# Kernel tuning notes

Measured on AMD Instinct MI355X. Metric: run time of the kernel, lower is better.

## Reference

```python
import jax, jax.numpy as jnp
import numpy as np

E, N, D = 800000, 50000, 64

def setup_inputs() -> dict:
    key = jax.random.key(0)
    k0, k1, k2, k3 = jax.random.split(key, 4)
    return {
        "edge_attrs": jax.random.normal(k0, (E, D), dtype=jnp.float32),
        "proj_W": jax.random.normal(k1, (D, D), dtype=jnp.float32) / np.float32(np.sqrt(D)),
        "proj_b": jnp.zeros((D,), dtype=jnp.float32),
        "upd_W": jax.random.normal(k2, (D, D), dtype=jnp.float32) / np.float32(np.sqrt(D)),
        "upd_b": jnp.zeros((D,), dtype=jnp.float32),
        "dst": jax.random.randint(k3, (E,), 0, N, dtype=jnp.int32),
        "n_nodes": N,
    }

def reference(edge_attrs, proj_W, proj_b, upd_W, upd_b, dst, n_nodes):
    # Project each edge attribute: node_projectors[e.type](e.data)
    proj = edge_attrs @ proj_W + proj_b                      # [E, D]
    # Mean-aggregate incoming edges per destination node (MeanAggregator)
    summed = jax.ops.segment_sum(proj, dst, num_segments=n_nodes)          # [N, D]
    counts = jax.ops.segment_sum(jnp.ones((dst.shape[0], 1), proj.dtype),
                                 dst, num_segments=n_nodes)                # [N, 1]
    aggregated = summed / jnp.maximum(counts, 1.0)           # nodes w/o edges -> 0
    # Per-node update: updaters(aggregated)
    return aggregated @ upd_W + upd_b                        # [N, D]
```

## Files before the change

kernel.cpp:

```cpp
#include <hip/hip_runtime.h>
#include <hip/hip_bf16.h>

#define D 64

__global__ void zero_kernel(int* __restrict__ p, int n) {
    int i = blockIdx.x * blockDim.x + threadIdx.x;
    if (i < n) p[i] = 0;
}

__global__ void count_kernel(const int* __restrict__ dst, int* __restrict__ counts, int E) {
    int e = blockIdx.x * blockDim.x + threadIdx.x;
    if (e < E) atomicAdd(&counts[dst[e]], 1);
}

__global__ void scan_kernel(const int* __restrict__ counts, int* __restrict__ offsets,
                            int* __restrict__ cursor, int N) {
    __shared__ int wsum[16];
    int t = threadIdx.x;
    int wave = t >> 6, lane = t & 63;
    int carry = 0;
    for (int base = 0; base < N; base += 1024) {
        int i = base + t;
        int v = (i < N) ? counts[i] : 0;
        int s = v;
        #pragma unroll
        for (int off = 1; off < 64; off <<= 1) {
            int x = __shfl_up(s, off);
            if (lane >= off) s += x;
        }
        if (lane == 63) wsum[wave] = s;
        __syncthreads();
        int wbase = 0, total = 0;
        #pragma unroll
        for (int w = 0; w < 16; ++w) {
            int x = wsum[w];
            total += x;
            if (w < wave) wbase += x;
        }
        int incl = s + wbase + carry;
        int excl = incl - v;
        if (i < N) { offsets[i] = excl; cursor[i] = excl; }
        carry += total;
        __syncthreads();
    }
    if (t == 0) offsets[N] = carry;
}

__global__ void fill_kernel(const int* __restrict__ dst, int* __restrict__ cursor,
                            int* __restrict__ csr, int E) {
    int e = blockIdx.x * blockDim.x + threadIdx.x;
    if (e < E) {
        int pos = atomicAdd(&cursor[dst[e]], 1);
        csr[pos] = e;
    }
}

__global__ void combine_kernel(const float* __restrict__ Wp, const float* __restrict__ Wu,
                               const float* __restrict__ bp, float* __restrict__ Wc,
                               float* __restrict__ bc) {
    int idx = blockIdx.x * blockDim.x + threadIdx.x;
    int d = idx >> 6, j = idx & 63;
    float s = 0.f;
    #pragma unroll
    for (int k = 0; k < D; ++k) s = fmaf(Wp[d * D + k], Wu[k * D + j], s);
    Wc[idx] = s;
    if (d == 0) {
        float t = 0.f;
        #pragma unroll
        for (int k = 0; k < D; ++k) t = fmaf(bp[k], Wu[k * D + j], t);
        bc[j] = t;
    }
}

__global__ __launch_bounds__(256) void node_kernel(
        const float* __restrict__ attrs, const int* __restrict__ csr,
        const int* __restrict__ offsets,
        const float* __restrict__ Wc, const float* __restrict__ bc,
        const float* __restrict__ ub, float* __restrict__ out, int N) {
    __shared__ float wlds[D * D];
    __shared__ float blds[D];
    __shared__ float ulds[D];
    int t = threadIdx.x;
    #pragma unroll
    for (int i = t; i < D * D; i += 256) wlds[i] = Wc[i];
    if (t < D) { blds[t] = bc[t]; ulds[t] = ub[t]; }
    __syncthreads();

    int wave = t >> 6, lane = t & 63;
    int n = blockIdx.x * 4 + wave;
    if (n >= N) return;

    int off = offsets[n];
    int cnt = offsets[n + 1] - off;

    float sum = 0.f;
    for (int base = 0; base < cnt; base += 64) {
        int m = cnt - base; if (m > 64) m = 64;
        int idxv = (lane < m) ? csr[off + base + lane] : 0;
        int jj = 0;
        for (; jj + 8 <= m; jj += 8) {
            int e0 = __shfl(idxv, jj + 0);
            int e1 = __shfl(idxv, jj + 1);
            int e2 = __shfl(idxv, jj + 2);
            int e3 = __shfl(idxv, jj + 3);
            int e4 = __shfl(idxv, jj + 4);
            int e5 = __shfl(idxv, jj + 5);
            int e6 = __shfl(idxv, jj + 6);
            int e7 = __shfl(idxv, jj + 7);
            float a0 = attrs[(size_t)e0 * D + lane];
            float a1 = attrs[(size_t)e1 * D + lane];
            float a2 = attrs[(size_t)e2 * D + lane];
            float a3 = attrs[(size_t)e3 * D + lane];
            float a4 = attrs[(size_t)e4 * D + lane];
            float a5 = attrs[(size_t)e5 * D + lane];
            float a6 = attrs[(size_t)e6 * D + lane];
            float a7 = attrs[(size_t)e7 * D + lane];
            sum += ((a0 + a1) + (a2 + a3)) + ((a4 + a5) + (a6 + a7));
        }
        for (; jj < m; ++jj) {
            int e = __shfl(idxv, jj);
            sum += attrs[(size_t)e * D + lane];
        }
    }

    float mean = (cnt > 0) ? sum / (float)cnt : 0.f;
    float acc = ulds[lane] + ((cnt > 0) ? blds[lane] : 0.f);
    #pragma unroll
    for (int d = 0; d < D; ++d) {
        float m = __shfl(mean, d);
        acc = fmaf(m, wlds[d * D + lane], acc);
    }
    out[(size_t)n * D + lane] = acc;
}

extern "C" void kernel_launch(void* const* d_in, const int* in_sizes, int n_in,
                              void* d_out, int out_size, void* d_ws, size_t ws_size,
                              hipStream_t stream) {
    const float* edge_attrs = (const float*)d_in[0];
    const float* proj_W     = (const float*)d_in[1];
    const float* proj_b     = (const float*)d_in[2];
    const float* upd_W      = (const float*)d_in[3];
    const float* upd_b      = (const float*)d_in[4];
    const int*   dst        = (const int*)d_in[5];

    const int E = in_sizes[0] / D;
    const int N = out_size / D;

    int*   counts  = (int*)d_ws;
    int*   offsets = counts + N;
    int*   cursor  = offsets + N + 1;
    int*   csr     = cursor + N;
    float* Wc      = (float*)(csr + E);
    float* bc      = Wc + D * D;

    zero_kernel<<<(N + 255) / 256, 256, 0, stream>>>(counts, N);

    int blocks_e = (E + 255) / 256;
    count_kernel<<<blocks_e, 256, 0, stream>>>(dst, counts, E);
    scan_kernel<<<1, 1024, 0, stream>>>(counts, offsets, cursor, N);
    fill_kernel<<<blocks_e, 256, 0, stream>>>(dst, cursor, csr, E);
    combine_kernel<<<16, 256, 0, stream>>>(proj_W, upd_W, proj_b, Wc, bc);

    int blocks_n = (N + 3) / 4;
    node_kernel<<<blocks_n, 256, 0, stream>>>(edge_attrs, csr, offsets,
                                              Wc, bc, upd_b, (float*)d_out, N);
}
```

Baseline: 211.4 us.

## Parallelize prefix scan across blocks and gather edges with float4 loads

The single-block serial scan over 50k counts becomes a three-kernel scheme: per-block sums, a scan of those block sums, then a per-block scan that adds the block offset. This spreads the scan across the GPU instead of running it as a long serial loop in one workgroup. The node gather now has each quarter-wave read a whole edge row as float4, so four edges are processed per iteration, and partial sums are combined with xor shuffles. The cost is two extra kernel launches and a cross-lane reduction, with no unroll-by-8 left in the gather.

```diff
diff --git a/kernel.cpp b/kernel.cpp
--- a/kernel.cpp
+++ b/kernel.cpp
@@ -13,37 +13,64 @@
     if (e < E) atomicAdd(&counts[dst[e]], 1);
 }
 
-__global__ void scan_kernel(const int* __restrict__ counts, int* __restrict__ offsets,
-                            int* __restrict__ cursor, int N) {
+__global__ void blocksum_kernel(const int* __restrict__ counts, int* __restrict__ bsums, int N) {
+    int t = threadIdx.x;
+    int i = blockIdx.x * 256 + t;
+    int v = (i < N) ? counts[i] : 0;
+    int lane = t & 63, wave = t >> 6;
+    #pragma unroll
+    for (int o = 1; o < 64; o <<= 1) v += __shfl_xor(v, o);
+    __shared__ int ws[4];
+    if (lane == 0) ws[wave] = v;
+    __syncthreads();
+    if (t == 0) bsums[blockIdx.x] = ws[0] + ws[1] + ws[2] + ws[3];
+}
+
+__global__ void blockscan_kernel(const int* __restrict__ bsums, int* __restrict__ boffs,
+                                 int* __restrict__ offsets, int N, int nb) {
     __shared__ int wsum[16];
     int t = threadIdx.x;
     int wave = t >> 6, lane = t & 63;
-    int carry = 0;
-    for (int base = 0; base < N; base += 1024) {
-        int i = base + t;
-        int v = (i < N) ? counts[i] : 0;
-        int s = v;
-        #pragma unroll
-        for (int off = 1; off < 64; off <<= 1) {
-            int x = __shfl_up(s, off);
-            if (lane >= off) s += x;
-        }
-        if (lane == 63) wsum[wave] = s;
-        __syncthreads();
-        int wbase = 0, total = 0;
-        #pragma unroll
-        for (int w = 0; w < 16; ++w) {
-            int x = wsum[w];
-            total += x;
-            if (w < wave) wbase += x;
-        }
-        int incl = s + wbase + carry;
-        int excl = incl - v;
-        if (i < N) { offsets[i] = excl; cursor[i] = excl; }
-        carry += total;
-        __syncthreads();
+    int v = (t < nb) ? bsums[t] : 0;
+    int s = v;
+    #pragma unroll
+    for (int off = 1; off < 64; off <<= 1) {
+        int x = __shfl_up(s, off);
+        if (lane >= off) s += x;
     }
-    if (t == 0) offsets[N] = carry;
+    if (lane == 63) wsum[wave] = s;
+    __syncthreads();
+    int wbase = 0, total = 0;
+    #pragma unroll
+    for (int w = 0; w < 16; ++w) {
+        int x = wsum[w];
+        total += x;
+        if (w < wave) wbase += x;
+    }
+    if (t < nb) boffs[t] = s - v + wbase;
+    if (t == 0) offsets[N] = total;
+}
+
+__global__ void scatter_scan_kernel(const int* __restrict__ counts, const int* __restrict__ boffs,
+                                    int* __restrict__ offsets, int* __restrict__ cursor, int N) {
+    int t = threadIdx.x;
+    int i = blockIdx.x * 256 + t;
+    int v = (i < N) ? counts[i] : 0;
+    int lane = t & 63, wave = t >> 6;
+    int s = v;
+    #pragma unroll
+    for (int off = 1; off < 64; off <<= 1) {
+        int x = __shfl_up(s, off);
+        if (lane >= off) s += x;
+    }
+    __shared__ int ws[4];
+    if (lane == 63) ws[wave] = s;
+    __syncthreads();
+    int wbase = 0;
+    #pragma unroll
+    for (int w = 0; w < 4; ++w) if (w < wave) wbase += ws[w];
+    int excl = s - v + wbase + boffs[blockIdx.x];
+    if (i < N) { offsets[i] = excl; cursor[i] = excl; }
 }
 
 __global__ void fill_kernel(const int* __restrict__ dst, int* __restrict__ cursor,
@@ -73,7 +100,7 @@
 }
 
 __global__ __launch_bounds__(256) void node_kernel(
-        const float* __restrict__ attrs, const int* __restrict__ csr,
+        const float4* __restrict__ attrs4, const int* __restrict__ csr,
         const int* __restrict__ offsets,
         const float* __restrict__ Wc, const float* __restrict__ bc,
         const float* __restrict__ ub, float* __restrict__ out, int N) {
@@ -93,44 +120,37 @@
     int off = offsets[n];
     int cnt = offsets[n + 1] - off;
 
-    float sum = 0.f;
+    int g = lane >> 4;
+    int q = lane & 15;
+
+    float4 acc = make_float4(0.f, 0.f, 0.f, 0.f);
     for (int base = 0; base < cnt; base += 64) {
         int m = cnt - base; if (m > 64) m = 64;
         int idxv = (lane < m) ? csr[off + base + lane] : 0;
-        int jj = 0;
-        for (; jj + 8 <= m; jj += 8) {
-            int e0 = __shfl(idxv, jj + 0);
-            int e1 = __shfl(idxv, jj + 1);
-            int e2 = __shfl(idxv, jj + 2);
-            int e3 = __shfl(idxv, jj + 3);
-            int e4 = __shfl(idxv, jj + 4);
-            int e5 = __shfl(idxv, jj + 5);
-            int e6 = __shfl(idxv, jj + 6);
-            int e7 = __shfl(idxv, jj + 7);
-            float a0 = attrs[(size_t)e0 * D + lane];
-            float a1 = attrs[(size_t)e1 * D + lane];
-            float a2 = attrs[(size_t)e2 * D + lane];
-            float a3 = attrs[(size_t)e3 * D + lane];
-            float a4 = attrs[(size_t)e4 * D + lane];
-            float a5 = attrs[(size_t)e5 * D + lane];
-            float a6 = attrs[(size_t)e6 * D + lane];
-            float a7 = attrs[(size_t)e7 * D + lane];
-            sum += ((a0 + a1) + (a2 + a3)) + ((a4 + a5) + (a6 + a7));
-        }
-        for (; jj < m; ++jj) {
-            int e = __shfl(idxv, jj);
-            sum += attrs[(size_t)e * D + lane];
+        for (int jj = 0; jj < m; jj += 4) {
+            int sel = jj + g;
+            int e = __shfl(idxv, sel);
+            if (sel < m) {
+                float4 a = attrs4[(size_t)e * 16 + q];
+                acc.x += a.x; acc.y += a.y; acc.z += a.z; acc.w += a.w;
+            }
         }
     }
+    acc.x += __shfl_xor(acc.x, 16); acc.y += __shfl_xor(acc.y, 16);
+    acc.z += __shfl_xor(acc.z, 16); acc.w += __shfl_xor(acc.w, 16);
+    acc.x += __shfl_xor(acc.x, 32); acc.y += __shfl_xor(acc.y, 32);
+    acc.z += __shfl_xor(acc.z, 32); acc.w += __shfl_xor(acc.w, 32);
 
-    float mean = (cnt > 0) ? sum / (float)cnt : 0.f;
-    float acc = ulds[lane] + ((cnt > 0) ? blds[lane] : 0.f);
+    float inv = (cnt > 0) ? 1.f / (float)cnt : 0.f;
+    float marr[4] = { acc.x * inv, acc.y * inv, acc.z * inv, acc.w * inv };
+
+    float accO = ulds[lane] + ((cnt > 0) ? blds[lane] : 0.f);
     #pragma unroll
     for (int d = 0; d < D; ++d) {
-        float m = __shfl(mean, d);
-        acc = fmaf(m, wlds[d * D + lane], acc);
+        float mv = __shfl(marr[d & 3], d >> 2);
+        accO = fmaf(mv, wlds[d * D + lane], accO);
     }
-    out[(size_t)n * D + lane] = acc;
+    out[(size_t)n * D + lane] = accO;
 }
 
 extern "C" void kernel_launch(void* const* d_in, const int* in_sizes, int n_in,
@@ -145,11 +165,14 @@
 
     const int E = in_sizes[0] / D;
     const int N = out_size / D;
+    const int nb = (N + 255) / 256;
 
     int*   counts  = (int*)d_ws;
     int*   offsets = counts + N;
     int*   cursor  = offsets + N + 1;
-    int*   csr     = cursor + N;
+    int*   bsums   = cursor + N;
+    int*   boffs   = bsums + nb;
+    int*   csr     = boffs + nb;
     float* Wc      = (float*)(csr + E);
     float* bc      = Wc + D * D;
 
@@ -157,11 +180,13 @@
 
     int blocks_e = (E + 255) / 256;
     count_kernel<<<blocks_e, 256, 0, stream>>>(dst, counts, E);
-    scan_kernel<<<1, 1024, 0, stream>>>(counts, offsets, cursor, N);
+    blocksum_kernel<<<nb, 256, 0, stream>>>(counts, bsums, N);
+    blockscan_kernel<<<1, 1024, 0, stream>>>(bsums, boffs, offsets, N, nb);
+    scatter_scan_kernel<<<nb, 256, 0, stream>>>(counts, boffs, offsets, cursor, N);
     fill_kernel<<<blocks_e, 256, 0, stream>>>(dst, cursor, csr, E);
     combine_kernel<<<16, 256, 0, stream>>>(proj_W, upd_W, proj_b, Wc, bc);
 
     int blocks_n = (N + 3) / 4;
-    node_kernel<<<blocks_n, 256, 0, stream>>>(edge_attrs, csr, offsets,
+    node_kernel<<<blocks_n, 256, 0, stream>>>((const float4*)edge_attrs, csr, offsets,
                                               Wc, bc, upd_b, (float*)d_out, N);
 }
```

New measurement: 171.3 us. 19.0% less time.
